# Kernel optimization log

Measured on AMD Instinct MI355X. Metric: run time of the kernel, lower is better.

## Reference

```python
import jax, jax.numpy as jnp
import numpy as np

B, SX, SY, D = 32, 2048, 2048, 160

def setup_inputs() -> dict:
    key = jax.random.key(0)
    ks = jax.random.split(key, 5)
    s = 1.0 / np.sqrt(D)
    return {
        "x": jax.random.normal(ks[0], (B, SX, D), dtype=jnp.float32),
        "y": jax.random.normal(ks[1], (B, SY, D), dtype=jnp.float32),
        "Wq": jax.random.normal(ks[2], (D, D), dtype=jnp.float32) * s,
        "bq": jnp.zeros((D,), dtype=jnp.float32),
        "Wk": jax.random.normal(ks[3], (D, D), dtype=jnp.float32) * s,
        "bk": jnp.zeros((D,), dtype=jnp.float32),
        "Wv": jax.random.normal(ks[4], (D, D), dtype=jnp.float32) * s,
        "bv": jnp.zeros((D,), dtype=jnp.float32),
    }

def reference(x, y, Wq, bq, Wk, bk, Wv, bv):
    # torch nn.Linear: out = in @ W.T + b, W is [out_dim, in_dim]
    q = jnp.einsum('bxd,ed->bxe', x, Wq) + bq          # [B,SX,D]
    k = jnp.einsum('byd,ed->bye', y, Wk) + bk          # [B,SY,D]
    v = jnp.einsum('byd,ed->bye', y, Wv) + bv          # [B,SY,D]
    scores = jnp.einsum('bxd,byd->bxy', q, k)          # [B,SX,SY] (no scaling in source)
    attn = jax.nn.softmax(scores, axis=-1)
    out = jnp.einsum('bxy,byd->bxd', attn, v)          # dropout is identity at eval
    return out + x                                     # residual
```

## Files before the change

### kernel.cpp

```cpp
#include <hip/hip_runtime.h>

#define LOG2E 1.44269504088896340736f

typedef _Float16 f16;
typedef __attribute__((ext_vector_type(2))) _Float16 f16x2;
typedef __attribute__((ext_vector_type(2))) __fp16 fp16x2;
typedef __attribute__((ext_vector_type(4))) _Float16 f16x4;
typedef __attribute__((ext_vector_type(8))) _Float16 f16x8;
typedef __attribute__((ext_vector_type(4))) float f32x4;
typedef __attribute__((ext_vector_type(16))) float f32x16;
typedef __attribute__((ext_vector_type(8))) unsigned short us8;
typedef __attribute__((ext_vector_type(2))) int i32x2;

#define BB 32
#define SSX 2048
#define SSY 2048
#define DD 160
#define M_TOTAL (BB*SSX)

#define PRS 168
#define VTRS 136
#define RS 168

__device__ __forceinline__ f32x4 mfma16(f16x8 a, f16x8 b, f32x4 c) {
  return __builtin_amdgcn_mfma_f32_16x16x32_f16(a, b, c, 0, 0, 0);
}

__device__ __forceinline__ f32x16 mfma32(f16x8 a, f16x8 b, f32x16 c) {
  return __builtin_amdgcn_mfma_f32_32x32x16_f16(a, b, c, 0, 0, 0);
}

__device__ __forceinline__ unsigned pk2rtz(float a, float b) {
  union { fp16x2 h; unsigned u; } x;
  x.h = __builtin_amdgcn_cvt_pkrtz(a, b);
  return x.u;
}

__global__ __launch_bounds__(256) void wcvt_kernel(
    const float* __restrict__ Wq, const float* __restrict__ Wk, const float* __restrict__ Wv,
    f16* __restrict__ Wf)
{
  int idx = blockIdx.x*256 + threadIdx.x;
  int which = idx / 6400;
  int off   = idx % 6400;
  const float* src = (which == 0) ? Wq : (which == 1 ? Wk : Wv);
  float4 v = *(const float4*)&src[off*4];
  f16x4 h = { (f16)v.x, (f16)v.y, (f16)v.z, (f16)v.w };
  *(f16x4*)&Wf[which*25600 + off*4] = h;
}

__global__ __launch_bounds__(256, 3) void proj_kernel(
    const float* __restrict__ x, const float* __restrict__ y,
    const float* __restrict__ bq, const float* __restrict__ bk, const float* __restrict__ bv,
    const f16* __restrict__ Wf,
    f16* __restrict__ Qw, f16* __restrict__ Kw, f16* __restrict__ Vtw)
{
  __shared__ __align__(16) f16 buf[160*PRS];
  const int t = threadIdx.x;
  const int wave = t >> 6;
  const int lane = t & 63;
  const int quad = lane >> 4;
  const int l16  = lane & 15;
  const int bid  = (blockIdx.x & 7) * 192 + (blockIdx.x >> 3);
  const int kind = bid % 3;
  const int tile = bid / 3;
  const int row0 = tile * 128;
  const float* src  = (kind == 0) ? x  : y;
  const f16*   W    = Wf + kind*25600;
  const float* bias = (kind == 0) ? bq : (kind == 1 ? bk : bv);

  #pragma unroll
  for (int i = 0; i < 12; ++i) {
    int idx = t + i*256;
    int r = idx / 20, g = idx % 20;
    *(us8*)&buf[r*PRS + g*8] = *(const us8*)&W[idx*8];
  }
  if (t < 128) {
    int idx = t + 3072;
    int r = idx / 20, g = idx % 20;
    *(us8*)&buf[r*PRS + g*8] = *(const us8*)&W[idx*8];
  }

  f16x8 afr0[5], afr1[5];
  {
    const float* r0p = src + (size_t)(row0 + wave*32 + l16)*DD;
    const float* r1p = r0p + 16*DD;
    #pragma unroll
    for (int ks = 0; ks < 5; ++ks) {
      float4 a = *(const float4*)&r0p[ks*32 + quad*8];
      float4 b = *(const float4*)&r0p[ks*32 + quad*8 + 4];
      afr0[ks] = (f16x8){(f16)a.x,(f16)a.y,(f16)a.z,(f16)a.w,
                         (f16)b.x,(f16)b.y,(f16)b.z,(f16)b.w};
      float4 c = *(const float4*)&r1p[ks*32 + quad*8];
      float4 d = *(const float4*)&r1p[ks*32 + quad*8 + 4];
      afr1[ks] = (f16x8){(f16)c.x,(f16)c.y,(f16)c.z,(f16)c.w,
                         (f16)d.x,(f16)d.y,(f16)d.z,(f16)d.w};
    }
  }
  __syncthreads();

  f32x4 acc0[10], acc1[10];
  #pragma unroll
  for (int nt = 0; nt < 10; ++nt) {
    float bs = bias[nt*16 + l16];
    acc0[nt] = (f32x4){bs,bs,bs,bs};
    acc1[nt] = (f32x4){bs,bs,bs,bs};
    #pragma unroll
    for (int ks = 0; ks < 5; ++ks) {
      f16x8 bfr = *(const f16x8*)&buf[(nt*16 + l16)*PRS + ks*32 + quad*8];
      acc0[nt] = mfma16(afr0[ks], bfr, acc0[nt]);
      acc1[nt] = mfma16(afr1[ks], bfr, acc1[nt]);
    }
  }
  __syncthreads();

  if (kind < 2) {
    f16* dst = (kind == 0) ? Qw : Kw;
    #pragma unroll
    for (int nt = 0; nt < 10; ++nt)
      #pragma unroll
      for (int r = 0; r < 4; ++r) {
        buf[(wave*32 + quad*4 + r)*PRS + nt*16 + l16]      = (f16)acc0[nt][r];
        buf[(wave*32 + 16 + quad*4 + r)*PRS + nt*16 + l16] = (f16)acc1[nt][r];
      }
    __syncthreads();
    for (int i = 0; i < 10; ++i) {
      int idx = t + i*256;
      int r = idx / 20, g = idx % 20;
      *(us8*)&dst[(size_t)(row0 + r)*DD + g*8] = *(const us8*)&buf[r*PRS + g*8];
    }
  } else {
    #pragma unroll
    for (int nt = 0; nt < 10; ++nt)
      #pragma unroll
      for (int r = 0; r < 4; ++r) {
        buf[(nt*16 + l16)*VTRS + wave*32 + quad*4 + r]      = (f16)acc0[nt][r];
        buf[(nt*16 + l16)*VTRS + wave*32 + 16 + quad*4 + r] = (f16)acc1[nt][r];
      }
    __syncthreads();
    const int b  = row0 / SSY;
    const int y0 = row0 % SSY;
    for (int i = 0; i < 10; ++i) {
      int idx = t + i*256;
      int d = idx / 16, yg = idx % 16;
      *(us8*)&Vtw[((size_t)b*DD + d)*SSY + y0 + yg*8] = *(const us8*)&buf[d*VTRS + yg*8];
    }
  }
}


#define LOAD_CHUNK(yb) { \
  const f16* ksrc = Kw + ((size_t)b*SSY + (yb))*DD; \
  const f16* vsrc = Vtw + (size_t)b*DD*SSY + (yb); \
  _Pragma("unroll") \
  for (int i = 0; i < 5; ++i) { \
    int idx = t + i*256; int r = idx/20, c = idx%20; \
    kreg[i] = *(const us8*)&ksrc[(size_t)r*DD + c*8]; \
  } \
  _Pragma("unroll") \
  for (int i = 0; i < 5; ++i) { \
    int idx = t + i*256; int d = idx>>3, g = idx&7; \
    vreg[i] = *(const us8*)&vsrc[(size_t)d*SSY + g*8]; \
  } \
}

#define STORE_CHUNK() { \
  _Pragma("unroll") \
  for (int i = 0; i < 5; ++i) { \
    int idx = t + i*256; int r = idx/20, c = idx%20; \
    *(us8*)&K_lds[r*RS + c*8] = kreg[i]; \
  } \
  _Pragma("unroll") \
  for (int i = 0; i < 5; ++i) { \
    int idx = t + i*256; int d = idx>>3, g = idx&7; \
    *(us8*)&Vt_lds[d*64 + ((g ^ (d & 7)) << 3)] = vreg[i]; \
  } \
}

__global__ __launch_bounds__(256, 2) void flash_kernel(
    const f16* __restrict__ Qw, const f16* __restrict__ Kw, const f16* __restrict__ Vtw,
    const float* __restrict__ x, float* __restrict__ out)
{
  __shared__ __align__(16) f16 K_lds[64*RS];
  __shared__ __align__(16) f16 Vt_lds[160*64];
  const int t = threadIdx.x;
  const int wave = t >> 6;
  const int lane = t & 63;
  const int l31  = lane & 31;
  const int hi   = lane >> 5;
  const int bid  = (blockIdx.x & 7) * 64 + (blockIdx.x >> 3);
  const int b    = bid >> 4;
  const int x0   = (bid & 15) * 128;

  us8 kreg[5], vreg[5];
  LOAD_CHUNK(0);

  f16x8 qfr[10];
  #pragma unroll
  for (int h = 0; h < 2; ++h) {
    if (h) __syncthreads();
    const f16* qsrc = Qw + ((size_t)b*SSX + x0 + h*64)*DD;
    for (int i = 0; i < 5; ++i) {
      int idx = t + i*256;
      int r = idx / 20, c = idx % 20;
      *(us8*)&K_lds[r*RS + c*8] = *(const us8*)&qsrc[(size_t)r*DD + c*8];
    }
    __syncthreads();
    if ((wave >> 1) == h) {
      const int base = (wave & 1)*32;
      #pragma unroll
      for (int s = 0; s < 10; ++s)
        qfr[s] = *(const f16x8*)&K_lds[(base + l31)*RS + s*16 + hi*8];
    }
  }

  f32x16 acc[5];
  #pragma unroll
  for (int i = 0; i < 5; ++i)
    #pragma unroll
    for (int r = 0; r < 16; ++r) acc[i][r] = 0.f;
  float m = -1e30f, l = 0.f;

  for (int yc = 0; yc < SSY/64; ++yc) {
    __syncthreads();
    STORE_CHUNK();
    __syncthreads();
    if (yc < SSY/64 - 1) LOAD_CHUNK((yc+1)*64);

    f32x16 S0, S1;
    #pragma unroll
    for (int r = 0; r < 16; ++r) { S0[r] = 0.f; S1[r] = 0.f; }
    __builtin_amdgcn_s_setprio(1);
    #pragma unroll
    for (int s = 0; s < 10; ++s) {
      f16x8 k0 = *(const f16x8*)&K_lds[l31*RS + s*16 + hi*8];
      f16x8 k1 = *(const f16x8*)&K_lds[(32 + l31)*RS + s*16 + hi*8];
      S0 = mfma32(k0, qfr[s], S0);
      S1 = mfma32(k1, qfr[s], S1);
    }
    __builtin_amdgcn_s_setprio(0);

    float pmax = fmaxf(S0[0], S0[1]);
    #pragma unroll
    for (int r = 2; r < 16; r += 2) pmax = fmaxf(fmaxf(pmax, S0[r]), S0[r+1]);
    #pragma unroll
    for (int r = 0; r < 16; r += 2) pmax = fmaxf(fmaxf(pmax, S1[r]), S1[r+1]);
    pmax = fmaxf(pmax, __shfl_xor(pmax, 32));

    if (__any(pmax > m + 8.f)) {
      float n  = fmaxf(m, pmax);
      float sc = exp2f((m - n)*LOG2E);
      m = n; l *= sc;
      #pragma unroll
      for (int r = 0; r < 16; ++r) {
        float scq = __shfl(sc, (r&3) + 8*(r>>2) + 4*hi);
        #pragma unroll
        for (int dt = 0; dt < 5; ++dt) acc[dt][r] *= scq;
      }
    }

    float lsum = 0.f;
    #pragma unroll
    for (int r = 0; r < 16; ++r) { S0[r] = exp2f((S0[r] - m)*LOG2E); lsum += S0[r]; }
    #pragma unroll
    for (int r = 0; r < 16; ++r) { S1[r] = exp2f((S1[r] - m)*LOG2E); lsum += S1[r]; }
    lsum += __shfl_xor(lsum, 32);
    l += lsum;

    #pragma unroll
    for (int c = 0; c < 4; ++c) {
      const int bo = (c & 1)*8;
      float s0 = (c < 2) ? S0[bo+0] : S1[bo+0];
      float s1 = (c < 2) ? S0[bo+1] : S1[bo+1];
      float s2 = (c < 2) ? S0[bo+2] : S1[bo+2];
      float s3 = (c < 2) ? S0[bo+3] : S1[bo+3];
      float s4 = (c < 2) ? S0[bo+4] : S1[bo+4];
      float s5 = (c < 2) ? S0[bo+5] : S1[bo+5];
      float s6 = (c < 2) ? S0[bo+6] : S1[bo+6];
      float s7 = (c < 2) ? S0[bo+7] : S1[bo+7];
      unsigned L0 = pk2rtz(s0, s1), L1 = pk2rtz(s2, s3);
      unsigned H0 = pk2rtz(s4, s5), H1 = pk2rtz(s6, s7);
      i32x2 r02 = __builtin_amdgcn_permlane32_swap((int)L0, (int)H0, false, false);
      i32x2 r13 = __builtin_amdgcn_permlane32_swap((int)L1, (int)H1, false, false);
      union { unsigned u[4]; f16x8 h; } ph;
      ph.u[0] = (unsigned)r02.x; ph.u[1] = (unsigned)r13.x;
      ph.u[2] = (unsigned)r02.y; ph.u[3] = (unsigned)r13.y;
      __builtin_amdgcn_s_setprio(1);
      #pragma unroll
      for (int dt = 0; dt < 5; ++dt) {
        int row = dt*32 + l31;
        f16x8 vf = *(const f16x8*)&Vt_lds[row*64 + (((c*2 + hi) ^ (row & 7)) << 3)];
        acc[dt] = mfma32(ph.h, vf, acc[dt]);
      }
      __builtin_amdgcn_s_setprio(0);
    }
  }

  #pragma unroll
  for (int r = 0; r < 16; ++r) {
    int qr = (r&3) + 8*(r>>2) + 4*hi;
    float rl = 1.f / __shfl(l, qr);
    size_t rowoff = ((size_t)b*SSX + x0 + wave*32 + qr)*DD + l31;
    #pragma unroll
    for (int dt = 0; dt < 5; ++dt) {
      size_t o = rowoff + (size_t)dt*32;
      out[o] = acc[dt][r]*rl + x[o];
    }
  }
}

extern "C" void kernel_launch(void* const* d_in, const int* in_sizes, int n_in,
                              void* d_out, int out_size, void* d_ws, size_t ws_size,
                              hipStream_t stream) {
  const float* x  = (const float*)d_in[0];
  const float* y  = (const float*)d_in[1];
  const float* Wq = (const float*)d_in[2];
  const float* bq = (const float*)d_in[3];
  const float* Wk = (const float*)d_in[4];
  const float* bk = (const float*)d_in[5];
  const float* Wv = (const float*)d_in[6];
  const float* bv = (const float*)d_in[7];

  f16* Qw  = (f16*)d_ws;
  f16* Kw  = Qw + (size_t)M_TOTAL*DD;
  f16* Vtw = Kw + (size_t)M_TOTAL*DD;
  size_t wf_off = (ws_size - 153600) & ~(size_t)255;
  f16* Wf = (f16*)((char*)d_ws + wf_off);

  wcvt_kernel<<<75, 256, 0, stream>>>(Wq, Wk, Wv, Wf);
  proj_kernel<<<1536, 256, 0, stream>>>(x, y, bq, bk, bv, Wf, Qw, Kw, Vtw);
  flash_kernel<<<512, 256, 0, stream>>>(Qw, Kw, Vtw, x, (float*)d_out);
}
```

Baseline: 281.8 us.

## Halve flash tiles to 64 query rows and 32-key chunks with 2-wave blocks

Shrinks each flash-attention block from 4 waves over 128 query rows to 2 waves over 64 rows and doubles the grid. The KV chunk goes from 64 to 32 keys, so each wave computes one S tile per iteration instead of two. The XOR swizzle on V^T in LDS is replaced by a padded row stride. The aim is smaller LDS and register use so more blocks fit per CU, at the cost of more loop iterations, more barriers per key and more global K/V reads per query row.

```diff
diff --git a/kernel.cpp b/kernel.cpp
--- a/kernel.cpp
+++ b/kernel.cpp
@@ -21,6 +21,8 @@
 #define PRS 168
 #define VTRS 136
 #define RS 168
+#define KVB 32
+#define VRS 40
 
 __device__ __forceinline__ f32x4 mfma16(f16x8 a, f16x8 b, f32x4 c) {
   return __builtin_amdgcn_mfma_f32_16x16x32_f16(a, b, c, 0, 0, 0);
@@ -154,12 +156,12 @@
   const f16* vsrc = Vtw + (size_t)b*DD*SSY + (yb); \
   _Pragma("unroll") \
   for (int i = 0; i < 5; ++i) { \
-    int idx = t + i*256; int r = idx/20, c = idx%20; \
+    int idx = t + i*128; int r = idx/20, c = idx%20; \
     kreg[i] = *(const us8*)&ksrc[(size_t)r*DD + c*8]; \
   } \
   _Pragma("unroll") \
   for (int i = 0; i < 5; ++i) { \
-    int idx = t + i*256; int d = idx>>3, g = idx&7; \
+    int idx = t + i*128; int d = idx>>2, g = idx&3; \
     vreg[i] = *(const us8*)&vsrc[(size_t)d*SSY + g*8]; \
   } \
 }
@@ -167,30 +169,30 @@
 #define STORE_CHUNK() { \
   _Pragma("unroll") \
   for (int i = 0; i < 5; ++i) { \
-    int idx = t + i*256; int r = idx/20, c = idx%20; \
+    int idx = t + i*128; int r = idx/20, c = idx%20; \
     *(us8*)&K_lds[r*RS + c*8] = kreg[i]; \
   } \
   _Pragma("unroll") \
   for (int i = 0; i < 5; ++i) { \
-    int idx = t + i*256; int d = idx>>3, g = idx&7; \
-    *(us8*)&Vt_lds[d*64 + ((g ^ (d & 7)) << 3)] = vreg[i]; \
+    int idx = t + i*128; int d = idx>>2, g = idx&3; \
+    *(us8*)&Vt_lds[d*VRS + g*8] = vreg[i]; \
   } \
 }
 
-__global__ __launch_bounds__(256, 2) void flash_kernel(
+__global__ __launch_bounds__(128, 2) void flash_kernel(
     const f16* __restrict__ Qw, const f16* __restrict__ Kw, const f16* __restrict__ Vtw,
     const float* __restrict__ x, float* __restrict__ out)
 {
-  __shared__ __align__(16) f16 K_lds[64*RS];
-  __shared__ __align__(16) f16 Vt_lds[160*64];
+  __shared__ __align__(16) f16 K_lds[KVB*RS];
+  __shared__ __align__(16) f16 Vt_lds[160*VRS];
   const int t = threadIdx.x;
   const int wave = t >> 6;
   const int lane = t & 63;
   const int l31  = lane & 31;
   const int hi   = lane >> 5;
-  const int bid  = (blockIdx.x & 7) * 64 + (blockIdx.x >> 3);
-  const int b    = bid >> 4;
-  const int x0   = (bid & 15) * 128;
+  const int bid  = (blockIdx.x & 7) * 128 + (blockIdx.x >> 3);
+  const int b    = bid >> 5;
+  const int x0   = (bid & 31) * 64;
 
   us8 kreg[5], vreg[5];
   LOAD_CHUNK(0);
@@ -199,18 +201,17 @@
   #pragma unroll
   for (int h = 0; h < 2; ++h) {
     if (h) __syncthreads();
-    const f16* qsrc = Qw + ((size_t)b*SSX + x0 + h*64)*DD;
+    const f16* qsrc = Qw + ((size_t)b*SSX + x0 + h*32)*DD;
     for (int i = 0; i < 5; ++i) {
-      int idx = t + i*256;
+      int idx = t + i*128;
       int r = idx / 20, c = idx % 20;
       *(us8*)&K_lds[r*RS + c*8] = *(const us8*)&qsrc[(size_t)r*DD + c*8];
     }
     __syncthreads();
-    if ((wave >> 1) == h) {
-      const int base = (wave & 1)*32;
+    if (wave == h) {
       #pragma unroll
       for (int s = 0; s < 10; ++s)
-        qfr[s] = *(const f16x8*)&K_lds[(base + l31)*RS + s*16 + hi*8];
+        qfr[s] = *(const f16x8*)&K_lds[l31*RS + s*16 + hi*8];
     }
   }
 
@@ -221,30 +222,26 @@
     for (int r = 0; r < 16; ++r) acc[i][r] = 0.f;
   float m = -1e30f, l = 0.f;
 
-  for (int yc = 0; yc < SSY/64; ++yc) {
+  for (int yc = 0; yc < SSY/KVB; ++yc) {
     __syncthreads();
     STORE_CHUNK();
     __syncthreads();
-    if (yc < SSY/64 - 1) LOAD_CHUNK((yc+1)*64);
-
-    f32x16 S0, S1;
-    #pragma unroll
-    for (int r = 0; r < 16; ++r) { S0[r] = 0.f; S1[r] = 0.f; }
+    if (yc < SSY/KVB - 1) LOAD_CHUNK((yc+1)*KVB);
+
+    f32x16 S0;
+    #pragma unroll
+    for (int r = 0; r < 16; ++r) S0[r] = 0.f;
     __builtin_amdgcn_s_setprio(1);
     #pragma unroll
     for (int s = 0; s < 10; ++s) {
       f16x8 k0 = *(const f16x8*)&K_lds[l31*RS + s*16 + hi*8];
-      f16x8 k1 = *(const f16x8*)&K_lds[(32 + l31)*RS + s*16 + hi*8];
       S0 = mfma32(k0, qfr[s], S0);
-      S1 = mfma32(k1, qfr[s], S1);
     }
     __builtin_amdgcn_s_setprio(0);
 
     float pmax = fmaxf(S0[0], S0[1]);
     #pragma unroll
     for (int r = 2; r < 16; r += 2) pmax = fmaxf(fmaxf(pmax, S0[r]), S0[r+1]);
-    #pragma unroll
-    for (int r = 0; r < 16; r += 2) pmax = fmaxf(fmaxf(pmax, S1[r]), S1[r+1]);
     pmax = fmaxf(pmax, __shfl_xor(pmax, 32));
 
     if (__any(pmax > m + 8.f)) {
@@ -262,24 +259,14 @@
     float lsum = 0.f;
     #pragma unroll
     for (int r = 0; r < 16; ++r) { S0[r] = exp2f((S0[r] - m)*LOG2E); lsum += S0[r]; }
-    #pragma unroll
-    for (int r = 0; r < 16; ++r) { S1[r] = exp2f((S1[r] - m)*LOG2E); lsum += S1[r]; }
     lsum += __shfl_xor(lsum, 32);
     l += lsum;
 
     #pragma unroll
-    for (int c = 0; c < 4; ++c) {
-      const int bo = (c & 1)*8;
-      float s0 = (c < 2) ? S0[bo+0] : S1[bo+0];
-      float s1 = (c < 2) ? S0[bo+1] : S1[bo+1];
-      float s2 = (c < 2) ? S0[bo+2] : S1[bo+2];
-      float s3 = (c < 2) ? S0[bo+3] : S1[bo+3];
-      float s4 = (c < 2) ? S0[bo+4] : S1[bo+4];
-      float s5 = (c < 2) ? S0[bo+5] : S1[bo+5];
-      float s6 = (c < 2) ? S0[bo+6] : S1[bo+6];
-      float s7 = (c < 2) ? S0[bo+7] : S1[bo+7];
-      unsigned L0 = pk2rtz(s0, s1), L1 = pk2rtz(s2, s3);
-      unsigned H0 = pk2rtz(s4, s5), H1 = pk2rtz(s6, s7);
+    for (int c = 0; c < 2; ++c) {
+      const int bo = c*8;
+      unsigned L0 = pk2rtz(S0[bo+0], S0[bo+1]), L1 = pk2rtz(S0[bo+2], S0[bo+3]);
+      unsigned H0 = pk2rtz(S0[bo+4], S0[bo+5]), H1 = pk2rtz(S0[bo+6], S0[bo+7]);
       i32x2 r02 = __builtin_amdgcn_permlane32_swap((int)L0, (int)H0, false, false);
       i32x2 r13 = __builtin_amdgcn_permlane32_swap((int)L1, (int)H1, false, false);
       union { unsigned u[4]; f16x8 h; } ph;
@@ -289,7 +276,7 @@
       #pragma unroll
       for (int dt = 0; dt < 5; ++dt) {
         int row = dt*32 + l31;
-        f16x8 vf = *(const f16x8*)&Vt_lds[row*64 + (((c*2 + hi) ^ (row & 7)) << 3)];
+        f16x8 vf = *(const f16x8*)&Vt_lds[row*VRS + (c*2 + hi)*8];
         acc[dt] = mfma32(ph.h, vf, acc[dt]);
       }
       __builtin_amdgcn_s_setprio(0);
@@ -329,5 +316,5 @@
 
   wcvt_kernel<<<75, 256, 0, stream>>>(Wq, Wk, Wv, Wf);
   proj_kernel<<<1536, 256, 0, stream>>>(x, y, bq, bk, bv, Wf, Qw, Kw, Vtw);
-  flash_kernel<<<512, 256, 0, stream>>>(Qw, Kw, Vtw, x, (float*)d_out);
-}
+  flash_kernel<<<1024, 128, 0, stream>>>(Qw, Kw, Vtw, x, (float*)d_out);
+}
```

Result: faster. 272.5 us (-3.3%).
